# Performance work log

Hardware: AMD Instinct MI355X
Metric: run time of the kernel (lower is better)

## Reference

```python
import jax, jax.numpy as jnp
import numpy as np

H = 64           # edge/node/global hidden size
IN_F = 4         # node_attr_size
OUT_F = 1        # out_size
NUM_EMB = 100    # edge_num_embeddings
SKIP = True


def setup_inputs() -> dict:
    key = jax.random.key(0)
    ks = jax.random.split(key, 24)
    T, N, E = 4, 20000, 320000
    NNZ = 340000
    inp = {
        'node_attr': jax.random.normal(ks[0], (T, N, IN_F), jnp.float32),
        'global_attr': jax.random.normal(ks[1], (1, H), jnp.float32),
        'L_values': jax.random.normal(ks[2], (NNZ,), jnp.float32),
        'coeff': jnp.ones((1,), jnp.float32),
        'edge_attr': jax.random.randint(ks[3], (T, E), 0, NUM_EMB),
        'edge_index': jax.random.randint(ks[4], (2, E), 0, N),
        'L_index': jax.random.randint(ks[5], (2, NNZ), 0, N),
        'num_processing_steps': 4,
        # parameters
        'emb': jax.random.normal(ks[6], (NUM_EMB, H), jnp.float32) * 0.05,
        'W_ne': jax.random.normal(ks[7], (IN_F, H), jnp.float32) * 0.1,
        'b_ne': jnp.zeros((H,), jnp.float32),
        'W_eb': jax.random.normal(ks[8], ((H + 2 * H) * 2 + H, H), jnp.float32) * 0.05,
        'b_eb': jnp.zeros((H,), jnp.float32),
        'W_nb': jax.random.normal(ks[9], (2 * H + 2 * H + H, H), jnp.float32) * 0.05,
        'b_nb': jnp.zeros((H,), jnp.float32),
        'W_gb': jax.random.normal(ks[10], (H + H + H, H), jnp.float32) * 0.05,
        'b_gb': jnp.zeros((H,), jnp.float32),
        'W_d1': jax.random.normal(ks[11], (H, H), jnp.float32) * 0.1,
        'b_d1': jnp.zeros((H,), jnp.float32),
        'W_d2': jax.random.normal(ks[12], (H, OUT_F), jnp.float32) * 0.1,
        'b_d2': jnp.zeros((OUT_F,), jnp.float32),
        'W_i1': jax.random.normal(ks[13], (H, H), jnp.float32) * 0.1,
        'b_i1': jnp.zeros((H,), jnp.float32),
        'W_i2': jax.random.normal(ks[14], (H, IN_F), jnp.float32) * 0.1,
        'b_i2': jnp.zeros((IN_F,), jnp.float32),
    }
    return inp


def reference(node_attr, global_attr, L_values, coeff, emb, W_ne, b_ne,
              W_eb, b_eb, W_nb, b_nb, W_gb, b_gb, W_d1, b_d1, W_d2, b_d2,
              W_i1, b_i1, W_i2, b_i2, edge_attr, edge_index, L_index,
              num_processing_steps):
    T, N, _ = node_attr.shape
    s, r = edge_index[0], edge_index[1]
    Li, Lj = L_index[0], L_index[1]

    # encoders (all T steps at once)
    x_enc = jax.nn.relu(node_attr @ W_ne + b_ne)   # [T,N,H]
    e_enc = emb[edge_attr]                         # [T,E,H]

    def laplacian(h):  # sparse sp_L @ h, h: [N,H]
        return jax.ops.segment_sum(L_values[:, None] * h[Lj], Li, num_segments=N)

    def step(carry, xe):
        h_x, h_e, h_g = carry
        x_t, e_t = xe
        node_cat = jnp.concatenate([x_t, h_x], axis=-1)          # [N,2H]
        edge_cat = jnp.concatenate([e_t, h_e], axis=-1)          # [E,2H]
        g = h_g[0]                                               # [H]
        E_ = edge_cat.shape[0]
        # EdgeBlock: edges + sender + receiver + globals
        eb_in = jnp.concatenate([edge_cat, node_cat[s], node_cat[r],
                                 jnp.broadcast_to(g, (E_, g.shape[0]))], axis=-1)
        e_new = jax.nn.relu(eb_in @ W_eb + b_eb)                 # [E,H]
        # NodeBlock: scatter_add aggregates of received/sent edges
        recv = jax.ops.segment_sum(e_new, r, num_segments=N)
        sent = jax.ops.segment_sum(e_new, s, num_segments=N)
        nb_in = jnp.concatenate([recv, sent, node_cat,
                                 jnp.broadcast_to(g, (N, g.shape[0]))], axis=-1)
        x_new = jax.nn.relu(nb_in @ W_nb + b_nb)                 # [N,H]
        # GlobalBlock: scatter_mean (single graph -> mean)
        gb_in = jnp.concatenate([e_new.mean(0), x_new.mean(0), g])[None]
        g_new = jax.nn.relu(gb_in @ W_gb + b_gb)                 # [1,H]
        h_x_next = h_x + x_new if SKIP else x_new
        time_d = h_x_next - h_x
        spat_d = coeff[0] * laplacian(h_x_next)  # pde='diff': coeff * L u
        return (h_x_next, e_new, g_new), (h_x_next, time_d, spat_d)

    h0 = (jnp.zeros((N, H), jnp.float32),
          jnp.zeros((e_enc.shape[1], H), jnp.float32),
          global_attr)
    _, (hid, time_d, spat_d) = jax.lax.scan(step, h0, (x_enc, e_enc))

    # decoders over all steps
    out_nodes = jax.nn.relu(hid @ W_d1 + b_d1) @ W_d2 + b_d2     # [T,N,OUT_F]
    pred_in = jax.nn.relu(hid @ W_i1 + b_i1) @ W_i2 + b_i2       # [T,N,IN_F]
    return out_nodes, time_d, spat_d, pred_in
```

## Files before the change

kernel.cpp:

```cpp
#include <hip/hip_runtime.h>

#define TT 4
#define NN 20000
#define EE 320000
#define NZ 340000

typedef __attribute__((ext_vector_type(8))) __bf16 bf16x8;
typedef __attribute__((ext_vector_type(16))) float f32x16;

__device__ __forceinline__ unsigned short f2bf(float f) {
    unsigned int u = __float_as_uint(f);
    u = (u + 0x7FFFu + ((u >> 16) & 1u)) >> 16;
    return (unsigned short)u;
}
__device__ __forceinline__ float bf2f(unsigned short h) {
    return __uint_as_float(((unsigned int)h) << 16);
}

#define GLL16(src, dst) __builtin_amdgcn_global_load_lds( \
    (const __attribute__((address_space(1))) unsigned int*)(src), \
    (__attribute__((address_space(3))) unsigned int*)(dst), 16, 0, 0)

__global__ void k_count(const int* __restrict__ r, const int* __restrict__ s,
                        const int* __restrict__ Li,
                        int* cnt_r, int* cnt_s, int* cnt_L) {
    int i = blockIdx.x * 256 + threadIdx.x;
    if (i < EE) { atomicAdd(&cnt_r[r[i]], 1); atomicAdd(&cnt_s[s[i]], 1); }
    if (i < NZ) { atomicAdd(&cnt_L[Li[i]], 1); }
}

__global__ __launch_bounds__(1024) void k_scan(int* cnt, int* rowp, int* wp) {
    int which = blockIdx.x;
    int* c = cnt + which * NN;
    int* row = rowp + which * (NN + 1);
    int* w = wp + which * NN;
    __shared__ int ssum[1024];
    int tid = threadIdx.x;
    const int CH = (NN + 1023) / 1024;
    int base = tid * CH;
    int s = 0;
    for (int i = 0; i < CH; ++i) { int idx = base + i; s += (idx < NN) ? c[idx] : 0; }
    ssum[tid] = s;
    __syncthreads();
    for (int o = 1; o < 1024; o <<= 1) {
        int v = (tid >= o) ? ssum[tid - o] : 0;
        __syncthreads();
        ssum[tid] += v;
        __syncthreads();
    }
    int run = (tid > 0) ? ssum[tid - 1] : 0;
    for (int i = 0; i < CH; ++i) {
        int idx = base + i;
        if (idx < NN) { row[idx] = run; w[idx] = run; run += c[idx]; }
    }
    if (tid == 1023) row[NN] = ssum[1023];
}

__global__ void k_scatter(const int* __restrict__ r, const int* __restrict__ s,
                          const int* __restrict__ Li, const int* __restrict__ Lj,
                          const float* __restrict__ Lv,
                          int* wp_r, int* wp_s, int* wp_L,
                          int* col_r, int* col_s, uint2* col_L8) {
    int i = blockIdx.x * 256 + threadIdx.x;
    if (i < EE) {
        col_r[atomicAdd(&wp_r[r[i]], 1)] = i;
        col_s[atomicAdd(&wp_s[s[i]], 1)] = i;
    }
    if (i < NZ) {
        int pos = atomicAdd(&wp_L[Li[i]], 1);
        uint2 v;
        v.x = (unsigned int)Lj[i];
        v.y = __float_as_uint(Lv[i]);
        col_L8[pos] = v;
    }
}

__global__ __launch_bounds__(256) void k_pack(
    const float* __restrict__ W_eb, const float* __restrict__ W_nb,
    const float* __restrict__ W_d1, const float* __restrict__ W_i1,
    const float* __restrict__ emb, unsigned short* __restrict__ Bpe,
    unsigned short* __restrict__ Bpu, unsigned short* __restrict__ Bpn,
    unsigned short* __restrict__ Bpd, unsigned short* __restrict__ emb_bf) {
    int t = blockIdx.x * 256 + threadIdx.x;
    if (t < 2 * 8 * 512) {
        int i = t & 7, l = (t >> 3) & 63, kb = (t >> 9) & 7, ch = t >> 12;
        int colv = ch * 32 + (l & 31);
        int k = kb * 16 + (l >> 5) * 8 + i;
        Bpe[t] = f2bf(W_eb[k * 64 + colv]);
    }
    if (t < 4 * 8 * 512) {
        int i = t & 7, l = (t >> 3) & 63, kb = (t >> 9) & 7, g = t >> 12;
        int colv = (g & 1) * 32 + (l & 31);
        int k = 128 + (g >> 1) * 128 + kb * 16 + (l >> 5) * 8 + i;
        Bpu[t] = f2bf(W_eb[k * 64 + colv]);
    }
    if (t < 2 * 16 * 512) {
        int i = t & 7, l = (t >> 3) & 63, kb = (t >> 9) % 16, ch = t / (16 * 512);
        int colv = ch * 32 + (l & 31);
        int k = kb * 16 + (l >> 5) * 8 + i;
        Bpn[t] = f2bf(W_nb[k * 64 + colv]);
    }
    if (t < 4 * 4 * 512) {
        int i = t & 7, l = (t >> 3) & 63, kb = (t >> 9) & 3, sec = t >> 11;
        int colv = (sec & 1) * 32 + (l & 31);
        int k = kb * 16 + (l >> 5) * 8 + i;
        const float* W = (sec < 2) ? W_d1 : W_i1;
        Bpd[t] = f2bf(W[k * 64 + colv]);
    }
    if (t < 100 * 64) emb_bf[t] = f2bf(emb[t]);
}

__global__ __launch_bounds__(256) void k_xenc(const float* __restrict__ na,
                                              const float* __restrict__ W_ne,
                                              const float* __restrict__ b_ne,
                                              unsigned short* __restrict__ xenc) {
    int row = blockIdx.x * 4 + (threadIdx.x >> 6);
    int j = threadIdx.x & 63;
    float4 a = *(const float4*)&na[(size_t)row * 4];
    float v = b_ne[j] + a.x * W_ne[j] + a.y * W_ne[64 + j] + a.z * W_ne[128 + j] + a.w * W_ne[192 + j];
    xenc[(size_t)row * 64 + j] = f2bf(fmaxf(v, 0.f));
}

__global__ void k_gbias(int do_update, const float* __restrict__ W_gb,
                        const float* __restrict__ b_gb, const float* __restrict__ W_eb,
                        const float* __restrict__ b_eb, const float* __restrict__ W_nb,
                        const float* __restrict__ b_nb, float* __restrict__ g_cur,
                        float* __restrict__ e_sum, float* __restrict__ x_sum,
                        float* __restrict__ gb_eb, float* __restrict__ gb_nb) {
    int j = threadIdx.x;
    float a = 0.f;
    if (do_update) {
        a = b_gb[j];
        for (int k = 0; k < 64; ++k) a += (e_sum[k] / (float)EE) * W_gb[k * 64 + j];
        for (int k = 0; k < 64; ++k) a += (x_sum[k] / (float)NN) * W_gb[(64 + k) * 64 + j];
        for (int k = 0; k < 64; ++k) a += g_cur[k] * W_gb[(128 + k) * 64 + j];
    }
    __syncthreads();
    if (do_update) {
        g_cur[j] = fmaxf(a, 0.f);
        e_sum[j] = 0.f;
        x_sum[j] = 0.f;
    }
    __syncthreads();
    float a1 = b_eb[j], a2 = b_nb[j];
    for (int k = 0; k < 64; ++k) {
        float gk = g_cur[k];
        a1 = fmaf(gk, W_eb[(384 + k) * 64 + j], a1);
        a2 = fmaf(gk, W_nb[(256 + k) * 64 + j], a2);
    }
    gb_eb[j] = a1;
    gb_nb[j] = a2;
}

__global__ __launch_bounds__(64) void k_usr(
    const unsigned short* __restrict__ xenc_t, const unsigned short* __restrict__ hx_bf,
    const unsigned short* __restrict__ Bpu, float2* __restrict__ usr) {
    const int ln = threadIdx.x;
    const int er = ln & 31, hi = ln >> 5;
    const int n0 = blockIdx.x * 32;
    const int n = n0 + er;

    f32x16 a0, a1, a2, a3;
    #pragma unroll
    for (int i = 0; i < 16; ++i) { a0[i] = 0.f; a1[i] = 0.f; a2[i] = 0.f; a3[i] = 0.f; }

    const unsigned short* sx = xenc_t + (size_t)64 * n + hi * 8;
    const unsigned short* sh = hx_bf + (size_t)64 * n + hi * 8;
    #pragma unroll
    for (int c = 0; c < 2; ++c) {
        const unsigned short* src = c ? sh : sx;
        #pragma unroll
        for (int kb = 0; kb < 4; ++kb) {
            bf16x8 a = *(const bf16x8*)(src + kb * 16);
            int kg = c * 4 + kb;
            bf16x8 b0 = *(const bf16x8*)&Bpu[(size_t)((0 * 8 + kg) * 64 + ln) * 8];
            bf16x8 b1 = *(const bf16x8*)&Bpu[(size_t)((1 * 8 + kg) * 64 + ln) * 8];
            bf16x8 b2 = *(const bf16x8*)&Bpu[(size_t)((2 * 8 + kg) * 64 + ln) * 8];
            bf16x8 b3 = *(const bf16x8*)&Bpu[(size_t)((3 * 8 + kg) * 64 + ln) * 8];
            a0 = __builtin_amdgcn_mfma_f32_32x32x16_bf16(a, b0, a0, 0, 0, 0);
            a1 = __builtin_amdgcn_mfma_f32_32x32x16_bf16(a, b1, a1, 0, 0, 0);
            a2 = __builtin_amdgcn_mfma_f32_32x32x16_bf16(a, b2, a2, 0, 0, 0);
            a3 = __builtin_amdgcn_mfma_f32_32x32x16_bf16(a, b3, a3, 0, 0, 0);
        }
    }
    #pragma unroll
    for (int r = 0; r < 16; ++r) {
        int row = (r & 3) + 8 * (r >> 2) + 4 * hi;
        size_t o = (size_t)(n0 + row) * 64;
        float2 vs = {a0[r], a1[r]};
        float2 vr = {a2[r], a3[r]};
        usr[o + er] = vs;
        usr[o + 32 + er] = vr;
    }
}

__global__ __launch_bounds__(512) void k_edge(
    unsigned short* __restrict__ h_e, const unsigned short* __restrict__ emb_bf,
    const float2* __restrict__ usr, const int* __restrict__ eattr_t,
    const int* __restrict__ sidx, const int* __restrict__ ridx,
    const unsigned short* __restrict__ Bp, const float* __restrict__ gbias,
    float* __restrict__ e_sum) {
    __shared__ unsigned short sBe[8192];
    __shared__ float sRed[8][64];
    const int tid = threadIdx.x;
    const int w = tid >> 6, ln = tid & 63;
    const int er = ln & 31, hi = ln >> 5;
    const int ebase = blockIdx.x * 256 + w * 32;
    const int e = ebase + er;

    const int siv = sidx[ebase + er];
    const int riv = ridx[ebase + er];
    const int ai = eattr_t[e];

    #pragma unroll
    for (int i = 0; i < 2; ++i) {
        int off = i * 4096 + w * 512;
        GLL16(Bp + off + ln * 8, sBe + off);
    }

    const unsigned short* s0 = emb_bf + (size_t)64 * ai + hi * 8;
    const unsigned short* s1 = h_e + (size_t)64 * e + hi * 8;
    bf16x8 a0 = *(const bf16x8*)(s0);
    bf16x8 a1 = *(const bf16x8*)(s0 + 16);
    bf16x8 a2 = *(const bf16x8*)(s0 + 32);
    bf16x8 a3 = *(const bf16x8*)(s0 + 48);
    bf16x8 a4 = *(const bf16x8*)(s1);
    bf16x8 a5 = *(const bf16x8*)(s1 + 16);
    bf16x8 a6 = *(const bf16x8*)(s1 + 32);
    bf16x8 a7 = *(const bf16x8*)(s1 + 48);

    f32x16 acc0, acc1;
    #pragma unroll
    for (int i = 0; i < 16; ++i) { acc0[i] = 0.f; acc1[i] = 0.f; }

    __syncthreads();

    #define EMM(AF, KG)                                                              \
        {                                                                            \
            bf16x8 b0 = *(const bf16x8*)&sBe[(((KG)) * 64 + ln) * 8];                \
            bf16x8 b1 = *(const bf16x8*)&sBe[((8 + (KG)) * 64 + ln) * 8];            \
            acc0 = __builtin_amdgcn_mfma_f32_32x32x16_bf16(AF, b0, acc0, 0, 0, 0);   \
            acc1 = __builtin_amdgcn_mfma_f32_32x32x16_bf16(AF, b1, acc1, 0, 0, 0);   \
        }
    EMM(a0, 0) EMM(a1, 1) EMM(a2, 2) EMM(a3, 3)
    EMM(a4, 4) EMM(a5, 5) EMM(a6, 6) EMM(a7, 7)
    #undef EMM

    const float gb0 = gbias[er], gb1 = gbias[er + 32];
    float cs0 = 0.f, cs1 = 0.f;
    #pragma unroll
    for (int r = 0; r < 16; ++r) {
        int row = (r & 3) + 8 * (r >> 2) + 4 * hi;
        int si_row = __shfl(siv, row, 64);
        int ri_row = __shfl(riv, row, 64);
        float2 us = usr[(size_t)si_row * 64 + er];
        float2 ur = usr[(size_t)ri_row * 64 + 32 + er];
        size_t o = (size_t)(ebase + row) * 64;
        float v0 = fmaxf(acc0[r] + us.x + ur.x + gb0, 0.f);
        float v1 = fmaxf(acc1[r] + us.y + ur.y + gb1, 0.f);
        cs0 += v0; cs1 += v1;
        h_e[o + er] = f2bf(v0);
        h_e[o + er + 32] = f2bf(v1);
    }
    cs0 += __shfl_xor(cs0, 32, 64);
    cs1 += __shfl_xor(cs1, 32, 64);
    if (hi == 0) { sRed[w][er] = cs0; sRed[w][er + 32] = cs1; }
    __syncthreads();
    if (w == 0) {
        float t = 0.f;
        #pragma unroll
        for (int q = 0; q < 8; ++q) t += sRed[q][ln];
        atomicAdd(&e_sum[ln], t);
    }
}

__global__ __launch_bounds__(256) void k_gather(
    const unsigned short* __restrict__ h_e, const int* __restrict__ row_r,
    const int* __restrict__ col_r, const int* __restrict__ row_s,
    const int* __restrict__ col_s, unsigned short* __restrict__ recv,
    unsigned short* __restrict__ sentb) {
    int t = blockIdx.x * 256 + threadIdx.x;
    int sub = t & 31, n = t >> 5;
    int g = sub & 15, which = sub >> 4;
    const int* rowp = which ? row_s : row_r;
    const int* colp = which ? col_s : col_r;
    unsigned short* outp = which ? sentb : recv;

    float a0 = 0.f, a1 = 0.f, a2 = 0.f, a3 = 0.f;
    int b0 = rowp[n], b1 = rowp[n + 1];
    for (int p = b0; p < b1; ++p) {
        uint2 v = *(const uint2*)&h_e[(size_t)64 * colp[p] + g * 4];
        a0 += bf2f((unsigned short)(v.x & 0xFFFF));
        a1 += bf2f((unsigned short)(v.x >> 16));
        a2 += bf2f((unsigned short)(v.y & 0xFFFF));
        a3 += bf2f((unsigned short)(v.y >> 16));
    }
    uint2 packed;
    packed.x = (unsigned int)f2bf(a0) | ((unsigned int)f2bf(a1) << 16);
    packed.y = (unsigned int)f2bf(a2) | ((unsigned int)f2bf(a3) << 16);
    *(uint2*)&outp[(size_t)64 * n + g * 4] = packed;
}

#define NODE_CHUNK(CIDX, BASE)                                                          \
    {                                                                                   \
        const unsigned short* src = (BASE) + hi * 8;                                    \
        _Pragma("unroll") for (int kb = 0; kb < 4; ++kb) {                              \
            bf16x8 a = *(const bf16x8*)(src + kb * 16);                                 \
            bf16x8 b0 = *(const bf16x8*)&Bp[(size_t)(((CIDX)*4 + kb) * 64 + ln) * 8];   \
            bf16x8 b1 = *(const bf16x8*)&Bp[(size_t)((16 + (CIDX)*4 + kb) * 64 + ln) * 8]; \
            acc0 = __builtin_amdgcn_mfma_f32_32x32x16_bf16(a, b0, acc0, 0, 0, 0);       \
            acc1 = __builtin_amdgcn_mfma_f32_32x32x16_bf16(a, b1, acc1, 0, 0, 0);       \
        }                                                                               \
    }

__global__ __launch_bounds__(64) void k_node(
    const unsigned short* __restrict__ recv, const unsigned short* __restrict__ sentb,
    const unsigned short* __restrict__ xenc_t, float* __restrict__ h_x,
    unsigned short* __restrict__ hx_bf, const unsigned short* __restrict__ Bp,
    const float* __restrict__ gbias, float* __restrict__ x_sum,
    unsigned short* __restrict__ hid_t, float* __restrict__ timed_t) {
    const int ln = threadIdx.x;
    const int er = ln & 31, hi = ln >> 5;
    const int n0 = blockIdx.x * 32;
    const int n = n0 + er;

    f32x16 acc0, acc1;
    #pragma unroll
    for (int i = 0; i < 16; ++i) { acc0[i] = 0.f; acc1[i] = 0.f; }

    NODE_CHUNK(0, recv + (size_t)64 * n)
    NODE_CHUNK(1, sentb + (size_t)64 * n)
    NODE_CHUNK(2, xenc_t + (size_t)64 * n)
    NODE_CHUNK(3, hx_bf + (size_t)64 * n)

    const float gb0 = gbias[er], gb1 = gbias[er + 32];
    float cs0 = 0.f, cs1 = 0.f;
    #pragma unroll
    for (int r = 0; r < 16; ++r) {
        int row = (r & 3) + 8 * (r >> 2) + 4 * hi;
        size_t o = (size_t)(n0 + row) * 64;
        float x0 = fmaxf(acc0[r] + gb0, 0.f);
        float x1 = fmaxf(acc1[r] + gb1, 0.f);
        cs0 += x0; cs1 += x1;
        float hx0 = h_x[o + er] + x0;
        float hx1 = h_x[o + er + 32] + x1;
        unsigned short hb0 = f2bf(hx0), hb1 = f2bf(hx1);
        h_x[o + er] = hx0;        h_x[o + er + 32] = hx1;
        hx_bf[o + er] = hb0;      hx_bf[o + er + 32] = hb1;
        hid_t[o + er] = hb0;      hid_t[o + er + 32] = hb1;
        timed_t[o + er] = x0;     timed_t[o + er + 32] = x1;
    }
    cs0 += __shfl_xor(cs0, 32, 64);
    cs1 += __shfl_xor(cs1, 32, 64);
    if (hi == 0) {
        atomicAdd(&x_sum[er], cs0);
        atomicAdd(&x_sum[er + 32], cs1);
    }
}

__global__ __launch_bounds__(256) void k_lap(
    const float* __restrict__ h_x, const int* __restrict__ row_L,
    const uint2* __restrict__ col_L8, const float* __restrict__ coeff,
    float* __restrict__ spat_t) {
    int t = blockIdx.x * 256 + threadIdx.x;
    int sub = t & 31, n = t >> 5;
    int g = sub & 15, half = sub >> 4;
    float a0 = 0.f, a1 = 0.f, a2 = 0.f, a3 = 0.f;
    int b0 = row_L[n], b1 = row_L[n + 1];
    int mid = b0 + ((b1 - b0) >> 1);
    int p0 = half ? mid : b0;
    int p1 = half ? b1 : mid;
    for (int p = p0; p < p1; ++p) {
        uint2 e = col_L8[p];
        float lv = __uint_as_float(e.y);
        float4 v = *(const float4*)&h_x[(size_t)64 * e.x + g * 4];
        a0 = fmaf(lv, v.x, a0);
        a1 = fmaf(lv, v.y, a1);
        a2 = fmaf(lv, v.z, a2);
        a3 = fmaf(lv, v.w, a3);
    }
    a0 += __shfl_xor(a0, 16, 64);
    a1 += __shfl_xor(a1, 16, 64);
    a2 += __shfl_xor(a2, 16, 64);
    a3 += __shfl_xor(a3, 16, 64);
    if (half == 0) {
        float c = coeff[0];
        float4 outv = {c * a0, c * a1, c * a2, c * a3};
        *(float4*)&spat_t[(size_t)64 * n + g * 4] = outv;
    }
}

__global__ __launch_bounds__(256) void k_dec(
    const unsigned short* __restrict__ hid_bf, const unsigned short* __restrict__ Bpd,
    const float* __restrict__ b_d1, const float* __restrict__ W_d2,
    const float* __restrict__ b_d2, const float* __restrict__ b_i1,
    const float* __restrict__ W_i2, const float* __restrict__ b_i2,
    float* __restrict__ out_nodes, float* __restrict__ pred_in) {
    __shared__ unsigned short sDec[4][32 * 138];
    const int tid = threadIdx.x;
    const int w = tid >> 6, ln = tid & 63;
    const int er = ln & 31, hi = ln >> 5;
    const int row0 = (blockIdx.x * 4 + w) * 32;

    f32x16 ad0, ad1, ai0, ai1;
    #pragma unroll
    for (int i = 0; i < 16; ++i) { ad0[i] = 0.f; ad1[i] = 0.f; ai0[i] = 0.f; ai1[i] = 0.f; }

    const unsigned short* src = hid_bf + (size_t)(row0 + er) * 64 + hi * 8;
    #pragma unroll
    for (int kb = 0; kb < 4; ++kb) {
        bf16x8 a = *(const bf16x8*)(src + kb * 16);
        bf16x8 bd0 = *(const bf16x8*)&Bpd[((0 * 4 + kb) * 64 + ln) * 8];
        bf16x8 bd1 = *(const bf16x8*)&Bpd[((4 + kb) * 64 + ln) * 8];
        bf16x8 bi0 = *(const bf16x8*)&Bpd[((8 + kb) * 64 + ln) * 8];
        bf16x8 bi1 = *(const bf16x8*)&Bpd[((12 + kb) * 64 + ln) * 8];
        ad0 = __builtin_amdgcn_mfma_f32_32x32x16_bf16(a, bd0, ad0, 0, 0, 0);
        ad1 = __builtin_amdgcn_mfma_f32_32x32x16_bf16(a, bd1, ad1, 0, 0, 0);
        ai0 = __builtin_amdgcn_mfma_f32_32x32x16_bf16(a, bi0, ai0, 0, 0, 0);
        ai1 = __builtin_amdgcn_mfma_f32_32x32x16_bf16(a, bi1, ai1, 0, 0, 0);
    }

    const float bd0v = b_d1[er], bd1v = b_d1[er + 32];
    const float bi0v = b_i1[er], bi1v = b_i1[er + 32];
    unsigned short* sw = &sDec[w][0];
    #pragma unroll
    for (int r = 0; r < 16; ++r) {
        int row = (r & 3) + 8 * (r >> 2) + 4 * hi;
        sw[row * 138 + er]       = f2bf(fmaxf(ad0[r] + bd0v, 0.f));
        sw[row * 138 + er + 32]  = f2bf(fmaxf(ad1[r] + bd1v, 0.f));
        sw[row * 138 + er + 64]  = f2bf(fmaxf(ai0[r] + bi0v, 0.f));
        sw[row * 138 + er + 96]  = f2bf(fmaxf(ai1[r] + bi1v, 0.f));
    }
    __syncthreads();

    const int g_row = row0 + er;
    if (hi == 0) {
        float s = 0.f;
        for (int k = 0; k < 32; ++k) {
            unsigned int u = *(const unsigned int*)&sw[er * 138 + 2 * k];
            s = fmaf(bf2f((unsigned short)(u & 0xFFFF)), W_d2[2 * k], s);
            s = fmaf(bf2f((unsigned short)(u >> 16)), W_d2[2 * k + 1], s);
        }
        out_nodes[g_row] = s + b_d2[0];
    } else {
        float s0 = 0.f, s1 = 0.f, s2 = 0.f, s3 = 0.f;
        for (int k = 0; k < 32; ++k) {
            unsigned int u = *(const unsigned int*)&sw[er * 138 + 64 + 2 * k];
            float vlo = bf2f((unsigned short)(u & 0xFFFF));
            float vhi = bf2f((unsigned short)(u >> 16));
            float4 w0 = *(const float4*)&W_i2[(2 * k) * 4];
            float4 w1 = *(const float4*)&W_i2[(2 * k + 1) * 4];
            s0 = fmaf(vlo, w0.x, fmaf(vhi, w1.x, s0));
            s1 = fmaf(vlo, w0.y, fmaf(vhi, w1.y, s1));
            s2 = fmaf(vlo, w0.z, fmaf(vhi, w1.z, s2));
            s3 = fmaf(vlo, w0.w, fmaf(vhi, w1.w, s3));
        }
        float4 pv = {s0 + b_i2[0], s1 + b_i2[1], s2 + b_i2[2], s3 + b_i2[3]};
        *(float4*)&pred_in[(size_t)4 * g_row] = pv;
    }
}

extern "C" void kernel_launch(void* const* d_in, const int* in_sizes, int n_in,
                              void* d_out, int out_size, void* d_ws, size_t ws_size,
                              hipStream_t stream) {
    (void)in_sizes; (void)n_in; (void)out_size; (void)ws_size;
    const float* node_attr   = (const float*)d_in[0];
    const float* global_attr = (const float*)d_in[1];
    const float* L_values    = (const float*)d_in[2];
    const float* coeff       = (const float*)d_in[3];
    const int*   edge_attr   = (const int*)d_in[4];
    const int*   edge_index  = (const int*)d_in[5];
    const int*   L_index     = (const int*)d_in[6];
    const float* emb  = (const float*)d_in[8];
    const float* W_ne = (const float*)d_in[9];
    const float* b_ne = (const float*)d_in[10];
    const float* W_eb = (const float*)d_in[11];
    const float* b_eb = (const float*)d_in[12];
    const float* W_nb = (const float*)d_in[13];
    const float* b_nb = (const float*)d_in[14];
    const float* W_gb = (const float*)d_in[15];
    const float* b_gb = (const float*)d_in[16];
    const float* W_d1 = (const float*)d_in[17];
    const float* b_d1 = (const float*)d_in[18];
    const float* W_d2 = (const float*)d_in[19];
    const float* b_d2 = (const float*)d_in[20];
    const float* W_i1 = (const float*)d_in[21];
    const float* b_i1 = (const float*)d_in[22];
    const float* W_i2 = (const float*)d_in[23];
    const float* b_i2 = (const float*)d_in[24];

    const int* s_idx = edge_index;
    const int* r_idx = edge_index + EE;
    const int* Li = L_index;
    const int* Lj = L_index + NZ;

    char* ws = (char*)d_ws;
    size_t off = 0;
    auto alloc = [&](size_t bytes) -> void* {
        void* p = ws + off;
        off = (off + bytes + 255) & ~(size_t)255;
        return p;
    };
    unsigned short* xenc   = (unsigned short*)alloc((size_t)TT * NN * 64 * 2);
    unsigned short* hid    = (unsigned short*)alloc((size_t)TT * NN * 64 * 2);
    float*          h_x    = (float*)alloc((size_t)NN * 64 * 4);
    unsigned short* hx_bf  = (unsigned short*)alloc((size_t)NN * 64 * 2);
    unsigned short* h_e    = (unsigned short*)alloc((size_t)EE * 64 * 2);
    unsigned short* recv   = (unsigned short*)alloc((size_t)NN * 64 * 2);
    unsigned short* sentb  = (unsigned short*)alloc((size_t)NN * 64 * 2);
    float2*         usr    = (float2*)alloc((size_t)NN * 64 * 8);
    float* smalls          = (float*)alloc(2048);
    unsigned short* Bpe    = (unsigned short*)alloc((size_t)2 * 8 * 512 * 2);
    unsigned short* Bpu    = (unsigned short*)alloc((size_t)4 * 8 * 512 * 2);
    unsigned short* Bpn    = (unsigned short*)alloc((size_t)2 * 16 * 512 * 2);
    unsigned short* Bpd    = (unsigned short*)alloc((size_t)4 * 4 * 512 * 2);
    unsigned short* emb_bf = (unsigned short*)alloc((size_t)100 * 64 * 2);
    int* cnt    = (int*)alloc((size_t)3 * NN * 4);
    int* rowp   = (int*)alloc((size_t)3 * (NN + 1) * 4);
    int* wp     = (int*)alloc((size_t)3 * NN * 4);
    int* col_r  = (int*)alloc((size_t)EE * 4);
    int* col_s  = (int*)alloc((size_t)EE * 4);
    uint2* col_L8 = (uint2*)alloc((size_t)NZ * 8);

    float* g_cur = smalls;
    float* e_sum = smalls + 64;
    float* x_sum = smalls + 128;
    float* gb_eb = smalls + 192;
    float* gb_nb = smalls + 256;
    int* cnt_r = cnt, *cnt_s = cnt + NN, *cnt_L = cnt + 2 * NN;
    int* row_r = rowp, *row_s = rowp + (NN + 1), *row_L = rowp + 2 * (NN + 1);
    int* wp_r = wp, *wp_s = wp + NN, *wp_L = wp + 2 * NN;

    float* out_nodes = (float*)d_out;
    float* time_d = out_nodes + (size_t)TT * NN;
    float* spat_d = time_d + (size_t)TT * NN * 64;
    float* pred_in = spat_d + (size_t)TT * NN * 64;

    hipMemsetAsync(h_x, 0, (size_t)NN * 64 * 4, stream);
    hipMemsetAsync(hx_bf, 0, (size_t)NN * 64 * 2, stream);
    hipMemsetAsync(h_e, 0, (size_t)EE * 64 * 2, stream);
    hipMemsetAsync(smalls, 0, 2048, stream);
    hipMemsetAsync(cnt, 0, (size_t)3 * NN * 4, stream);
    hipMemcpyAsync(g_cur, global_attr, 64 * 4, hipMemcpyDeviceToDevice, stream);

    k_count<<<(NZ + 255) / 256, 256, 0, stream>>>(r_idx, s_idx, Li, cnt_r, cnt_s, cnt_L);
    k_scan<<<3, 1024, 0, stream>>>(cnt, rowp, wp);
    k_scatter<<<(NZ + 255) / 256, 256, 0, stream>>>(r_idx, s_idx, Li, Lj, L_values,
                                                    wp_r, wp_s, wp_L,
                                                    col_r, col_s, col_L8);
    k_pack<<<96, 256, 0, stream>>>(W_eb, W_nb, W_d1, W_i1, emb,
                                   Bpe, Bpu, Bpn, Bpd, emb_bf);
    k_xenc<<<TT * NN / 4, 256, 0, stream>>>(node_attr, W_ne, b_ne, xenc);
    k_gbias<<<1, 64, 0, stream>>>(0, W_gb, b_gb, W_eb, b_eb, W_nb, b_nb,
                                  g_cur, e_sum, x_sum, gb_eb, gb_nb);

    for (int t = 0; t < TT; ++t) {
        const unsigned short* xenc_t = xenc + (size_t)t * NN * 64;
        k_usr<<<NN / 32, 64, 0, stream>>>(xenc_t, hx_bf, Bpu, usr);
        k_edge<<<EE / 256, 512, 0, stream>>>(h_e, emb_bf, usr,
                                             edge_attr + (size_t)t * EE, s_idx, r_idx,
                                             Bpe, gb_eb, e_sum);
        k_gather<<<NN * 32 / 256, 256, 0, stream>>>(h_e, row_r, col_r, row_s, col_s,
                                                    recv, sentb);
        k_node<<<NN / 32, 64, 0, stream>>>(recv, sentb, xenc_t, h_x, hx_bf,
                                           Bpn, gb_nb, x_sum,
                                           hid + (size_t)t * NN * 64,
                                           time_d + (size_t)t * NN * 64);
        k_lap<<<NN * 32 / 256, 256, 0, stream>>>(h_x, row_L, col_L8, coeff,
                                                 spat_d + (size_t)t * NN * 64);
        k_gbias<<<1, 64, 0, stream>>>(1, W_gb, b_gb, W_eb, b_eb, W_nb, b_nb,
                                      g_cur, e_sum, x_sum, gb_eb, gb_nb);
    }
    k_dec<<<TT * NN / 128, 256, 0, stream>>>(hid, Bpd, b_d1, W_d2, b_d2,
                                             b_i1, W_i2, b_i2, out_nodes, pred_in);
}
```

Before: 755.0 us.

## Fold global-bias kernel into k_usr, skip zero edge state at t=0, bf16 laplacian

Removes the separate single-block k_gbias launches by computing the global update and bias vectors inside block 0 of k_usr. At t=0 the edge kernel skips loading and multiplying the all-zero previous edge state, which also drops the 41 MB h_e memset. The laplacian now gathers the bf16 copy of h_x instead of fp32, halving gather bytes but lowering precision of spat_d. The fused bias is written by block 0 while other blocks of k_usr don't read it, so ordering holds via the next launch.

```diff
diff --git a/kernel.cpp b/kernel.cpp
--- a/kernel.cpp
+++ b/kernel.cpp
@@ -121,42 +121,41 @@
     xenc[(size_t)row * 64 + j] = f2bf(fmaxf(v, 0.f));
 }
 
-__global__ void k_gbias(int do_update, const float* __restrict__ W_gb,
-                        const float* __restrict__ b_gb, const float* __restrict__ W_eb,
-                        const float* __restrict__ b_eb, const float* __restrict__ W_nb,
-                        const float* __restrict__ b_nb, float* __restrict__ g_cur,
-                        float* __restrict__ e_sum, float* __restrict__ x_sum,
-                        float* __restrict__ gb_eb, float* __restrict__ gb_nb) {
-    int j = threadIdx.x;
-    float a = 0.f;
-    if (do_update) {
-        a = b_gb[j];
-        for (int k = 0; k < 64; ++k) a += (e_sum[k] / (float)EE) * W_gb[k * 64 + j];
-        for (int k = 0; k < 64; ++k) a += (x_sum[k] / (float)NN) * W_gb[(64 + k) * 64 + j];
-        for (int k = 0; k < 64; ++k) a += g_cur[k] * W_gb[(128 + k) * 64 + j];
-    }
-    __syncthreads();
-    if (do_update) {
-        g_cur[j] = fmaxf(a, 0.f);
-        e_sum[j] = 0.f;
-        x_sum[j] = 0.f;
-    }
-    __syncthreads();
-    float a1 = b_eb[j], a2 = b_nb[j];
-    for (int k = 0; k < 64; ++k) {
-        float gk = g_cur[k];
-        a1 = fmaf(gk, W_eb[(384 + k) * 64 + j], a1);
-        a2 = fmaf(gk, W_nb[(256 + k) * 64 + j], a2);
-    }
-    gb_eb[j] = a1;
-    gb_nb[j] = a2;
-}
-
 __global__ __launch_bounds__(64) void k_usr(
+    int do_update,
     const unsigned short* __restrict__ xenc_t, const unsigned short* __restrict__ hx_bf,
-    const unsigned short* __restrict__ Bpu, float2* __restrict__ usr) {
+    const unsigned short* __restrict__ Bpu, float2* __restrict__ usr,
+    const float* __restrict__ W_gb, const float* __restrict__ b_gb,
+    const float* __restrict__ W_eb, const float* __restrict__ b_eb,
+    const float* __restrict__ W_nb, const float* __restrict__ b_nb,
+    float* __restrict__ g_cur, float* __restrict__ e_sum, float* __restrict__ x_sum,
+    float* __restrict__ gb_eb, float* __restrict__ gb_nb) {
     const int ln = threadIdx.x;
     const int er = ln & 31, hi = ln >> 5;
+
+    if (blockIdx.x == 0) {
+        int j = ln;
+        float gv = g_cur[j];
+        if (do_update) {
+            float a = b_gb[j];
+            for (int k = 0; k < 64; ++k) a += (e_sum[k] / (float)EE) * W_gb[k * 64 + j];
+            for (int k = 0; k < 64; ++k) a += (x_sum[k] / (float)NN) * W_gb[(64 + k) * 64 + j];
+            for (int k = 0; k < 64; ++k) a += g_cur[k] * W_gb[(128 + k) * 64 + j];
+            gv = fmaxf(a, 0.f);
+            g_cur[j] = gv;
+            e_sum[j] = 0.f;
+            x_sum[j] = 0.f;
+        }
+        float a1 = b_eb[j], a2 = b_nb[j];
+        for (int k = 0; k < 64; ++k) {
+            float gk = __shfl(gv, k, 64);
+            a1 = fmaf(gk, W_eb[(384 + k) * 64 + j], a1);
+            a2 = fmaf(gk, W_nb[(256 + k) * 64 + j], a2);
+        }
+        gb_eb[j] = a1;
+        gb_nb[j] = a2;
+    }
+
     const int n0 = blockIdx.x * 32;
     const int n = n0 + er;
 
@@ -195,7 +194,8 @@
 }
 
 __global__ __launch_bounds__(512) void k_edge(
-    unsigned short* __restrict__ h_e, const unsigned short* __restrict__ emb_bf,
+    int first, unsigned short* __restrict__ h_e,
+    const unsigned short* __restrict__ emb_bf,
     const float2* __restrict__ usr, const int* __restrict__ eattr_t,
     const int* __restrict__ sidx, const int* __restrict__ ridx,
     const unsigned short* __restrict__ Bp, const float* __restrict__ gbias,
@@ -224,10 +224,13 @@
     bf16x8 a1 = *(const bf16x8*)(s0 + 16);
     bf16x8 a2 = *(const bf16x8*)(s0 + 32);
     bf16x8 a3 = *(const bf16x8*)(s0 + 48);
-    bf16x8 a4 = *(const bf16x8*)(s1);
-    bf16x8 a5 = *(const bf16x8*)(s1 + 16);
-    bf16x8 a6 = *(const bf16x8*)(s1 + 32);
-    bf16x8 a7 = *(const bf16x8*)(s1 + 48);
+    bf16x8 a4{}, a5{}, a6{}, a7{};
+    if (!first) {
+        a4 = *(const bf16x8*)(s1);
+        a5 = *(const bf16x8*)(s1 + 16);
+        a6 = *(const bf16x8*)(s1 + 32);
+        a7 = *(const bf16x8*)(s1 + 48);
+    }
 
     f32x16 acc0, acc1;
     #pragma unroll
@@ -243,7 +246,9 @@
             acc1 = __builtin_amdgcn_mfma_f32_32x32x16_bf16(AF, b1, acc1, 0, 0, 0);   \
         }
     EMM(a0, 0) EMM(a1, 1) EMM(a2, 2) EMM(a3, 3)
-    EMM(a4, 4) EMM(a5, 5) EMM(a6, 6) EMM(a7, 7)
+    if (!first) {
+        EMM(a4, 4) EMM(a5, 5) EMM(a6, 6) EMM(a7, 7)
+    }
     #undef EMM
 
     const float gb0 = gbias[er], gb1 = gbias[er + 32];
@@ -359,7 +364,7 @@
 }
 
 __global__ __launch_bounds__(256) void k_lap(
-    const float* __restrict__ h_x, const int* __restrict__ row_L,
+    const unsigned short* __restrict__ hx_bf, const int* __restrict__ row_L,
     const uint2* __restrict__ col_L8, const float* __restrict__ coeff,
     float* __restrict__ spat_t) {
     int t = blockIdx.x * 256 + threadIdx.x;
@@ -373,11 +378,11 @@
     for (int p = p0; p < p1; ++p) {
         uint2 e = col_L8[p];
         float lv = __uint_as_float(e.y);
-        float4 v = *(const float4*)&h_x[(size_t)64 * e.x + g * 4];
-        a0 = fmaf(lv, v.x, a0);
-        a1 = fmaf(lv, v.y, a1);
-        a2 = fmaf(lv, v.z, a2);
-        a3 = fmaf(lv, v.w, a3);
+        uint2 hv = *(const uint2*)&hx_bf[(size_t)64 * e.x + g * 4];
+        a0 = fmaf(lv, bf2f((unsigned short)(hv.x & 0xFFFF)), a0);
+        a1 = fmaf(lv, bf2f((unsigned short)(hv.x >> 16)), a1);
+        a2 = fmaf(lv, bf2f((unsigned short)(hv.y & 0xFFFF)), a2);
+        a3 = fmaf(lv, bf2f((unsigned short)(hv.y >> 16)), a3);
     }
     a0 += __shfl_xor(a0, 16, 64);
     a1 += __shfl_xor(a1, 16, 64);
@@ -538,7 +543,6 @@
 
     hipMemsetAsync(h_x, 0, (size_t)NN * 64 * 4, stream);
     hipMemsetAsync(hx_bf, 0, (size_t)NN * 64 * 2, stream);
-    hipMemsetAsync(h_e, 0, (size_t)EE * 64 * 2, stream);
     hipMemsetAsync(smalls, 0, 2048, stream);
     hipMemsetAsync(cnt, 0, (size_t)3 * NN * 4, stream);
     hipMemcpyAsync(g_cur, global_attr, 64 * 4, hipMemcpyDeviceToDevice, stream);
@@ -551,13 +555,13 @@
     k_pack<<<96, 256, 0, stream>>>(W_eb, W_nb, W_d1, W_i1, emb,
                                    Bpe, Bpu, Bpn, Bpd, emb_bf);
     k_xenc<<<TT * NN / 4, 256, 0, stream>>>(node_attr, W_ne, b_ne, xenc);
-    k_gbias<<<1, 64, 0, stream>>>(0, W_gb, b_gb, W_eb, b_eb, W_nb, b_nb,
-                                  g_cur, e_sum, x_sum, gb_eb, gb_nb);
 
     for (int t = 0; t < TT; ++t) {
         const unsigned short* xenc_t = xenc + (size_t)t * NN * 64;
-        k_usr<<<NN / 32, 64, 0, stream>>>(xenc_t, hx_bf, Bpu, usr);
-        k_edge<<<EE / 256, 512, 0, stream>>>(h_e, emb_bf, usr,
+        k_usr<<<NN / 32, 64, 0, stream>>>(t > 0, xenc_t, hx_bf, Bpu, usr,
+                                          W_gb, b_gb, W_eb, b_eb, W_nb, b_nb,
+                                          g_cur, e_sum, x_sum, gb_eb, gb_nb);
+        k_edge<<<EE / 256, 512, 0, stream>>>(t == 0, h_e, emb_bf, usr,
                                              edge_attr + (size_t)t * EE, s_idx, r_idx,
                                              Bpe, gb_eb, e_sum);
         k_gather<<<NN * 32 / 256, 256, 0, stream>>>(h_e, row_r, col_r, row_s, col_s,
@@ -566,10 +570,8 @@
                                            Bpn, gb_nb, x_sum,
                                            hid + (size_t)t * NN * 64,
                                            time_d + (size_t)t * NN * 64);
-        k_lap<<<NN * 32 / 256, 256, 0, stream>>>(h_x, row_L, col_L8, coeff,
+        k_lap<<<NN * 32 / 256, 256, 0, stream>>>(hx_bf, row_L, col_L8, coeff,
                                                  spat_d + (size_t)t * NN * 64);
-        k_gbias<<<1, 64, 0, stream>>>(1, W_gb, b_gb, W_eb, b_eb, W_nb, b_nb,
-                                      g_cur, e_sum, x_sum, gb_eb, gb_nb);
     }
     k_dec<<<TT * NN / 128, 256, 0, stream>>>(hid, Bpd, b_d1, W_d2, b_d2,
                                              b_i1, W_i2, b_i2, out_nodes, pred_in);
```

Result: faster. 695.7 us (-7.9%).
